# Performance work log

Hardware: AMD Instinct MI355X
Metric: run time of the kernel (lower is better)

Reference implementation:

```python
import jax, jax.numpy as jnp
import numpy as np

TOPK = 7  # hard-coded k in cal_high_score_instance_mask
EPS_DICE = 1e-8


def setup_inputs() -> dict:
    key = jax.random.key(0)
    k1, k2, k3, k4 = jax.random.split(key, 4)
    b, n, v, h, w = 4, 16, 32, 160, 160
    pred_mask = jax.random.normal(k1, (b, 1, h, w), dtype=jnp.float32)
    encode_feat = jax.random.normal(k2, (b, v, h, w), dtype=jnp.float32)
    gt_instances = (jax.random.uniform(k3, (b, n, h, w)) > 0.8).astype(jnp.float32)
    # validity mask over instance slots
    gt_index_mask = jax.random.randint(k4, (b, n), 0, 2).astype(jnp.int32)
    return {
        "pred_mask": pred_mask,
        "encode_feat": encode_feat,
        "gt_instances": gt_instances,
        "gt_index_mask": gt_index_mask,
    }


def reference(pred_mask, encode_feat, gt_instances, gt_index_mask):
    b, v, h, w = encode_feat.shape
    n = gt_instances.shape[1]
    hw = h * w
    feat = encode_feat.reshape(b, v, hw)          # b, v, hw
    gt = gt_instances.reshape(b, n, hw)           # b, n, hw
    valid = gt_index_mask.astype(feat.dtype)      # b, n  (0/1)

    # ---- get_mean_embedding_vector: masked mean of embedding per instance
    pix = jnp.clip(gt.sum(-1), 1.0)               # b, n
    mean_emb = jnp.einsum('bvp,bnp->bnv', feat, gt) / pix[..., None]

    # ---- cal_high_score_instance_mask: topk over masked score map, gather embeddings
    pre_regions = pred_mask.reshape(b, 1, hw) * gt             # b, n, hw
    _wvals, idx = jax.lax.top_k(pre_regions, TOPK)              # b, n, k
    idx_flat = idx.reshape(b, n * TOPK)                         # b, n*k
    # gather embedding vectors at topk pixel locations -> b, n*k, v
    idx_feat_th = jnp.take_along_axis(feat, idx_flat[:, None, :], axis=2)
    idx_feat_th = jnp.transpose(idx_feat_th, (0, 2, 1))

    # ---- get_isntance_mask: embedding-vector x feature-map matmuls
    inst_masks = jnp.einsum('bkv,bvp->bkp', idx_feat_th, feat)  # b, n*k, hw
    mean_masks = jnp.einsum('bnv,bvp->bnp', mean_emb, feat)     # b, n, hw

    # ---- w_dice_loss on mean-embedding masks (valid instances only)
    p_mean = jax.nn.sigmoid(mean_masks)
    denom_mean = jnp.clip((p_mean ** 2).sum(-1) + (gt ** 2).sum(-1), EPS_DICE)
    dice_mean = 1.0 - 2.0 * (gt * p_mean).sum(-1) / denom_mean  # b, n
    mean_inst_loss = (dice_mean * valid).sum()

    # ---- w_dice_loss on topk-instance masks (target expanded over k)
    p_k = jax.nn.sigmoid(inst_masks.reshape(b, n, TOPK, hw))
    t_k = gt[:, :, None, :]                                     # b, n, 1, hw
    denom_k = jnp.clip((p_k ** 2).sum(-1) + (t_k ** 2).sum(-1), EPS_DICE)
    dice_k = 1.0 - 2.0 * (t_k * p_k).sum(-1) / denom_k          # b, n, k
    inst_loss = (dice_k * valid[..., None]).sum()

    # ---- l2_loss: masked squared distance of per-pixel embedding to instance mean
    diff = (feat[:, None, :, :] - mean_emb[..., None]) * gt[:, :, None, :]  # b, n, v, hw
    l2 = (diff ** 2).sum(-1) / pix[..., None]                   # b, n, v
    embedding_l2_loss = (l2.sum(-1) * valid).sum()

    return jnp.stack([mean_inst_loss, inst_loss, embedding_l2_loss])
```

## Files before the change

### kernel.cpp

```cpp
#include <hip/hip_runtime.h>
#include <cstdint>
#include <cstddef>

#define B 4
#define N 16
#define V 32
#define HW 25600
#define TOPK 7
#define NSLB 5
#define NCA 200
#define NCC 400

__device__ __forceinline__ bool better(float av, int ai, float bv, int bi) {
    return (av > bv) || (av == bv && ai < bi);
}

__global__ __launch_bounds__(256) void kTop(
    const float* __restrict__ pred, const float* __restrict__ gt,
    float* __restrict__ cand_val, int* __restrict__ cand_idx,
    float* __restrict__ cnt_part, float* __restrict__ out) {
    int s = blockIdx.x;
    int tid = threadIdx.x;
    if (s == 0 && tid == 0) { out[0] = 0.f; out[1] = 0.f; out[2] = 0.f; }
    int bn = s / NSLB, sl = s % NSLB;
    int b = bn >> 4;
    int lane = tid & 63, wave = tid >> 6;
    int base = sl * 5120;

    const float* gtrow = gt + (size_t)bn * HW + base;
    const float* pr = pred + (size_t)b * HW + base;

    float tv[TOPK]; int ti[TOPK];
#pragma unroll
    for (int j = 0; j < TOPK; ++j) { tv[j] = -INFINITY; ti[j] = 0x7fffffff; }
    float cnt = 0.f;

#pragma unroll
    for (int it = 0; it < 5; ++it) {
        int p = it * 1024 + tid * 4;
        float4 g4 = *reinterpret_cast<const float4*>(gtrow + p);
        float4 p4 = *reinterpret_cast<const float4*>(pr + p);
        cnt += g4.x + g4.y + g4.z + g4.w;
        float ca[4] = { p4.x * g4.x, p4.y * g4.y, p4.z * g4.z, p4.w * g4.w };
#pragma unroll
        for (int j = 0; j < 4; ++j) {
            float c = ca[j]; int pi = base + p + j;
            if (better(c, pi, tv[TOPK - 1], ti[TOPK - 1])) {
                tv[TOPK - 1] = c; ti[TOPK - 1] = pi;
#pragma unroll
                for (int q = TOPK - 2; q >= 0; --q) {
                    if (better(tv[q + 1], ti[q + 1], tv[q], ti[q])) {
                        float fv = tv[q]; int fi = ti[q];
                        tv[q] = tv[q + 1]; ti[q] = ti[q + 1];
                        tv[q + 1] = fv; ti[q + 1] = fi;
                    }
                }
            }
        }
    }

    __shared__ float rwv[4];
    __shared__ int rwi[4];
    __shared__ float csum[4];

#pragma unroll
    for (int off = 32; off > 0; off >>= 1) cnt += __shfl_down(cnt, off);
    if (lane == 0) csum[wave] = cnt;
    __syncthreads();
    if (tid == 0) cnt_part[s] = csum[0] + csum[1] + csum[2] + csum[3];

    int cbase = s * TOPK;
    for (int r = 0; r < TOPK; ++r) {
        float bv = tv[0]; int bi = ti[0];
#pragma unroll
        for (int m = 1; m <= 32; m <<= 1) {
            float ov = __shfl_xor(bv, m);
            int oi = __shfl_xor(bi, m);
            if (better(ov, oi, bv, bi)) { bv = ov; bi = oi; }
        }
        if (lane == 0) { rwv[wave] = bv; rwi[wave] = bi; }
        __syncthreads();
        float fv = rwv[0]; int fi = rwi[0];
#pragma unroll
        for (int w = 1; w < 4; ++w)
            if (better(rwv[w], rwi[w], fv, fi)) { fv = rwv[w]; fi = rwi[w]; }
        if (ti[0] == fi) {
#pragma unroll
            for (int q = 0; q < TOPK - 1; ++q) { tv[q] = tv[q + 1]; ti[q] = ti[q + 1]; }
            tv[TOPK - 1] = -INFINITY; ti[TOPK - 1] = 0x7fffffff;
        }
        if (tid == 0) { cand_val[cbase + r] = fv; cand_idx[cbase + r] = fi; }
        __syncthreads();
    }
}

__global__ __launch_bounds__(256) void kA(
    const float* __restrict__ feat, const float* __restrict__ gt,
    float* __restrict__ ms_part, float* __restrict__ s2_part) {
    int s = blockIdx.x;
    int xcd = s & 7;
    int b = xcd >> 1;
    int ch = (s >> 3) * 2 + (xcd & 1);
    int c0 = ch * 128;
    int tid = threadIdx.x;
    int ng = tid >> 6, vg = (tid >> 3) & 7, pg = tid & 7;

    const float* gb = gt + (size_t)(b * N + ng * 4) * HW + c0 + pg * 4;
    const float* fb = feat + (size_t)(b * V + vg * 4) * HW + c0 + pg * 4;

    float acc[4][4];
#pragma unroll
    for (int i = 0; i < 4; ++i)
#pragma unroll
        for (int j = 0; j < 4; ++j) acc[i][j] = 0.f;
    float s2a[4] = { 0.f, 0.f, 0.f, 0.f };

#pragma unroll
    for (int q = 0; q < 4; ++q) {
        int p = q * 32;
        float4 g4[4], f4[4];
#pragma unroll
        for (int i = 0; i < 4; ++i)
            g4[i] = *reinterpret_cast<const float4*>(gb + (size_t)i * HW + p);
#pragma unroll
        for (int j = 0; j < 4; ++j)
            f4[j] = *reinterpret_cast<const float4*>(fb + (size_t)j * HW + p);
        float ffx = 0.f, ffy = 0.f, ffz = 0.f, ffw = 0.f;
#pragma unroll
        for (int j = 0; j < 4; ++j) {
            ffx = fmaf(f4[j].x, f4[j].x, ffx);
            ffy = fmaf(f4[j].y, f4[j].y, ffy);
            ffz = fmaf(f4[j].z, f4[j].z, ffz);
            ffw = fmaf(f4[j].w, f4[j].w, ffw);
        }
#pragma unroll
        for (int i = 0; i < 4; ++i) {
#pragma unroll
            for (int j = 0; j < 4; ++j) {
                acc[i][j] = fmaf(g4[i].x, f4[j].x, acc[i][j]);
                acc[i][j] = fmaf(g4[i].y, f4[j].y, acc[i][j]);
                acc[i][j] = fmaf(g4[i].z, f4[j].z, acc[i][j]);
                acc[i][j] = fmaf(g4[i].w, f4[j].w, acc[i][j]);
            }
            s2a[i] = fmaf(g4[i].x, ffx, s2a[i]);
            s2a[i] = fmaf(g4[i].y, ffy, s2a[i]);
            s2a[i] = fmaf(g4[i].z, ffz, s2a[i]);
            s2a[i] = fmaf(g4[i].w, ffw, s2a[i]);
        }
    }
#pragma unroll
    for (int m = 1; m <= 4; m <<= 1)
#pragma unroll
        for (int i = 0; i < 4; ++i)
#pragma unroll
            for (int j = 0; j < 4; ++j) acc[i][j] += __shfl_xor(acc[i][j], m);
    size_t blk = (size_t)(b * NCA + ch);
    if (pg == 0) {
        float* dst = ms_part + blk * 512;
#pragma unroll
        for (int i = 0; i < 4; ++i)
#pragma unroll
            for (int j = 0; j < 4; ++j)
                dst[(ng * 4 + i) * 32 + vg * 4 + j] = acc[i][j];
    }
#pragma unroll
    for (int m = 1; m <= 32; m <<= 1)
#pragma unroll
        for (int i = 0; i < 4; ++i) s2a[i] += __shfl_xor(s2a[i], m);
    if ((tid & 63) == 0) {
#pragma unroll
        for (int i = 0; i < 4; ++i)
            s2_part[blk * 16 + ng * 4 + i] = s2a[i];
    }
}

__global__ __launch_bounds__(256) void kB(
    const float* __restrict__ feat, const float* __restrict__ ms_part,
    const float* __restrict__ s2_part,
    const float* __restrict__ cand_val, const int* __restrict__ cand_idx,
    const float* __restrict__ cnt_part, const int* __restrict__ valid,
    float* __restrict__ Ebuf, float* __restrict__ cntbuf, float* __restrict__ out) {
    int bn = blockIdx.x;
    int b = bn >> 4, n = bn & 15;
    int tid = threadIdx.x;
    int lane = tid & 63, wave = tid >> 6;

    __shared__ float msl[8][33];
    __shared__ float s2w[4];
    __shared__ int idx7[TOPK];

    {
        int sl = tid >> 5, v = tid & 31;
        const float* src = ms_part + ((size_t)(b * NCA) + sl) * 512 + n * 32 + v;
        float sm = 0.f;
#pragma unroll 5
        for (int k = 0; k < 25; ++k) sm += src[(size_t)(8 * k) * 512];
        msl[sl][v] = sm;
    }
    {
        float s2v = 0.f;
        if (tid < NCA) s2v = s2_part[((size_t)(b * NCA) + tid) * 16 + n];
#pragma unroll
        for (int m = 1; m <= 32; m <<= 1) s2v += __shfl_xor(s2v, m);
        if (lane == 0) s2w[wave] = s2v;
    }
    if (wave == 0) {
        float cv = -INFINITY; int ci = 0x7fffffff;
        if (lane < NSLB * TOPK) {
            cv = cand_val[(size_t)bn * NSLB * TOPK + lane];
            ci = cand_idx[(size_t)bn * NSLB * TOPK + lane];
        }
#pragma unroll
        for (int r = 0; r < TOPK; ++r) {
            float bv = cv; int bi = ci;
#pragma unroll
            for (int m = 1; m <= 32; m <<= 1) {
                float ov = __shfl_xor(bv, m);
                int oi = __shfl_xor(bi, m);
                if (better(ov, oi, bv, bi)) { bv = ov; bi = oi; }
            }
            if (ci == bi) { cv = -INFINITY; ci = 0x7fffffff; }
            if (lane == 0) idx7[r] = bi;
        }
    }
    __syncthreads();

    if (tid < 32) {
        const float* cp = cnt_part + bn * NSLB;
        float cnt = cp[0] + cp[1] + cp[2] + cp[3] + cp[4];
        float msum = msl[0][tid] + msl[1][tid] + msl[2][tid] + msl[3][tid]
                   + msl[4][tid] + msl[5][tid] + msl[6][tid] + msl[7][tid];
        float pix = fmaxf(cnt, 1.0f);
        float mu = msum / pix;
        Ebuf[(size_t)bn * 256 + tid] = mu;
        float msq = mu * mu;
#pragma unroll
        for (int m = 1; m <= 16; m <<= 1) msq += __shfl_xor(msq, m);
        if (tid == 0) {
            cntbuf[bn] = cnt;
            float s2 = s2w[0] + s2w[1] + s2w[2] + s2w[3];
            atomicAdd(out + 2, (s2 / pix - msq) * (float)valid[bn]);
        }
    } else {
        int t = tid - 32;
        if (t < 224) {
            int r = t >> 5, v = t & 31;
            Ebuf[(size_t)bn * 256 + (r + 1) * 32 + v] =
                feat[((size_t)b * V + v) * HW + idx7[r]];
        }
    }
}

__global__ __launch_bounds__(256) void kC(
    const float* __restrict__ feat, const float* __restrict__ gt,
    const float* __restrict__ Ebuf, float* __restrict__ sums_part) {
    int s = blockIdx.x;
    int xcd = s & 7;
    int b = xcd >> 1;
    int ch = (s >> 3) * 2 + (xcd & 1);
    int c0 = ch * 64;
    int tid = threadIdx.x;
    int n = tid >> 4, pg = tid & 15;

    __shared__ float e_lds[8 * 16 * 36];
    __shared__ float red[16][17];

    const float* eb = Ebuf + (size_t)b * 4096;
#pragma unroll
    for (int k = 0; k < 4; ++k) {
        int q = (tid + 256 * k) * 4;
        int nn = q >> 8, rr = (q >> 5) & 7, vv = q & 31;
        *reinterpret_cast<float4*>(&e_lds[(rr * 16 + nn) * 36 + vv]) =
            *reinterpret_cast<const float4*>(eb + q);
    }
    __syncthreads();

    const float* fb = feat + (size_t)b * V * HW + c0 + pg * 4;
    float4 g4 = *reinterpret_cast<const float4*>(gt + (size_t)(b * N + n) * HW + c0 + pg * 4);

    float acc[8][4];
#pragma unroll
    for (int r = 0; r < 8; ++r)
#pragma unroll
        for (int j = 0; j < 4; ++j) acc[r][j] = 0.f;

    float4 c0_ = *reinterpret_cast<const float4*>(fb);
    float4 c1_ = *reinterpret_cast<const float4*>(fb + HW);
    float4 c2_ = *reinterpret_cast<const float4*>(fb + 2 * (size_t)HW);
    float4 c3_ = *reinterpret_cast<const float4*>(fb + 3 * (size_t)HW);
#pragma unroll
    for (int vq = 0; vq < 8; ++vq) {
        float4 n0_, n1_, n2_, n3_;
        if (vq < 7) {
            const float* np = fb + (size_t)(vq * 4 + 4) * HW;
            n0_ = *reinterpret_cast<const float4*>(np);
            n1_ = *reinterpret_cast<const float4*>(np + HW);
            n2_ = *reinterpret_cast<const float4*>(np + 2 * (size_t)HW);
            n3_ = *reinterpret_cast<const float4*>(np + 3 * (size_t)HW);
        }
#pragma unroll
        for (int r = 0; r < 8; ++r) {
            float4 e4 = *reinterpret_cast<const float4*>(&e_lds[(r * 16 + n) * 36 + vq * 4]);
            acc[r][0] = fmaf(e4.x, c0_.x, acc[r][0]);
            acc[r][0] = fmaf(e4.y, c1_.x, acc[r][0]);
            acc[r][0] = fmaf(e4.z, c2_.x, acc[r][0]);
            acc[r][0] = fmaf(e4.w, c3_.x, acc[r][0]);
            acc[r][1] = fmaf(e4.x, c0_.y, acc[r][1]);
            acc[r][1] = fmaf(e4.y, c1_.y, acc[r][1]);
            acc[r][1] = fmaf(e4.z, c2_.y, acc[r][1]);
            acc[r][1] = fmaf(e4.w, c3_.y, acc[r][1]);
            acc[r][2] = fmaf(e4.x, c0_.z, acc[r][2]);
            acc[r][2] = fmaf(e4.y, c1_.z, acc[r][2]);
            acc[r][2] = fmaf(e4.z, c2_.z, acc[r][2]);
            acc[r][2] = fmaf(e4.w, c3_.z, acc[r][2]);
            acc[r][3] = fmaf(e4.x, c0_.w, acc[r][3]);
            acc[r][3] = fmaf(e4.y, c1_.w, acc[r][3]);
            acc[r][3] = fmaf(e4.z, c2_.w, acc[r][3]);
            acc[r][3] = fmaf(e4.w, c3_.w, acc[r][3]);
        }
        if (vq < 7) { c0_ = n0_; c1_ = n1_; c2_ = n2_; c3_ = n3_; }
    }

    float p2[8], tp[8];
#pragma unroll
    for (int r = 0; r < 8; ++r) { p2[r] = 0.f; tp[r] = 0.f; }
    float ga[4] = { g4.x, g4.y, g4.z, g4.w };
#pragma unroll
    for (int r = 0; r < 8; ++r)
#pragma unroll
        for (int j = 0; j < 4; ++j) {
            float sg = 1.f / (1.f + __expf(-acc[r][j]));
            p2[r] = fmaf(sg, sg, p2[r]);
            tp[r] = fmaf(ga[j], sg, tp[r]);
        }
#pragma unroll
    for (int m = 1; m <= 8; m <<= 1)
#pragma unroll
        for (int r = 0; r < 8; ++r) {
            p2[r] += __shfl_xor(p2[r], m);
            tp[r] += __shfl_xor(tp[r], m);
        }
    if (pg == 0) {
#pragma unroll
        for (int r = 0; r < 8; ++r) {
            red[n][r * 2] = p2[r];
            red[n][r * 2 + 1] = tp[r];
        }
    }
    __syncthreads();
    sums_part[(size_t)(b * NCC + ch) * 256 + tid] = red[tid >> 4][tid & 15];
}

__global__ __launch_bounds__(256) void kD(
    const float* __restrict__ sums_part, const float* __restrict__ cntbuf,
    const int* __restrict__ valid, float* __restrict__ out) {
    int bn = blockIdx.x;
    int b = bn >> 4, n = bn & 15;
    int tid = threadIdx.x;
    int slot = tid & 15, cg = tid >> 4;
    int lane = tid & 63, wave = tid >> 6;

    __shared__ float red2[4][17];
    __shared__ float fin[16];

    float sv = 0.f;
    const float* src = sums_part + (size_t)b * NCC * 256 + n * 16 + slot;
    for (int k = 0; k < 25; ++k) sv += src[(size_t)(cg + 16 * k) * 256];
    sv += __shfl_xor(sv, 16);
    sv += __shfl_xor(sv, 32);
    if (lane < 16) red2[wave][lane] = sv;
    __syncthreads();
    if (tid < 16) fin[tid] = red2[0][tid] + red2[1][tid] + red2[2][tid] + red2[3][tid];
    __syncthreads();

    if (tid == 0) {
        float vw = (float)valid[bn];
        float cnt = cntbuf[bn];
        float mloss = 0.f, iloss = 0.f;
#pragma unroll
        for (int r = 0; r < 8; ++r) {
            float p2 = fin[r * 2];
            float tp = fin[r * 2 + 1];
            float denom = fmaxf(p2 + cnt, 1e-8f);
            float dice = 1.f - 2.f * tp / denom;
            if (r == 0) mloss = dice * vw;
            else iloss += dice * vw;
        }
        atomicAdd(out + 0, mloss);
        atomicAdd(out + 1, iloss);
    }
}

extern "C" void kernel_launch(void* const* d_in, const int* in_sizes, int n_in,
                              void* d_out, int out_size, void* d_ws, size_t ws_size,
                              hipStream_t stream) {
    const float* pred = (const float*)d_in[0];
    const float* feat = (const float*)d_in[1];
    const float* gtin = (const float*)d_in[2];
    const int* valid  = (const int*)d_in[3];
    float* out = (float*)d_out;

    char* ws = (char*)d_ws;
    float* ms_part   = (float*)(ws);
    float* s2_part   = (float*)(ws + 1638400);
    float* cand_val  = (float*)(ws + 1689600);
    int*   cand_idx  = (int*)  (ws + 1698560);
    float* cnt_part  = (float*)(ws + 1707520);
    float* sums_part = (float*)(ws + 1708800);
    float* Ebuf      = (float*)(ws + 3347200);
    float* cntbuf    = (float*)(ws + 3412736);

    kTop<<<B * N * NSLB, 256, 0, stream>>>(pred, gtin, cand_val, cand_idx, cnt_part, out);
    kA<<<B * NCA, 256, 0, stream>>>(feat, gtin, ms_part, s2_part);
    kB<<<B * N, 256, 0, stream>>>(feat, ms_part, s2_part, cand_val, cand_idx,
                                  cnt_part, valid, Ebuf, cntbuf, out);
    kC<<<B * NCC, 256, 0, stream>>>(feat, gtin, Ebuf, sums_part);
    kD<<<B * N, 256, 0, stream>>>(sums_part, cntbuf, valid, out);
}
```

Measured before the change: 63.40 us.

## Merge five kernels into one cooperative persistent kernel with grid syncs

```diff
diff --git a/kernel.cpp b/kernel.cpp
--- a/kernel.cpp
+++ b/kernel.cpp
@@ -1,6 +1,9 @@
 #include <hip/hip_runtime.h>
+#include <hip/hip_cooperative_groups.h>
 #include <cstdint>
 #include <cstddef>
+
+namespace cg = cooperative_groups;
 
 #define B 4
 #define N 16
@@ -10,19 +13,20 @@
 #define NSLB 5
 #define NCA 200
 #define NCC 400
+#define GRID 512
 
 __device__ __forceinline__ bool better(float av, int ai, float bv, int bi) {
     return (av > bv) || (av == bv && ai < bi);
 }
 
-__global__ __launch_bounds__(256) void kTop(
+
+__device__ __forceinline__ void kTop_body(
+    int slab, int tid,
     const float* __restrict__ pred, const float* __restrict__ gt,
     float* __restrict__ cand_val, int* __restrict__ cand_idx,
-    float* __restrict__ cnt_part, float* __restrict__ out) {
-    int s = blockIdx.x;
-    int tid = threadIdx.x;
-    if (s == 0 && tid == 0) { out[0] = 0.f; out[1] = 0.f; out[2] = 0.f; }
-    int bn = s / NSLB, sl = s % NSLB;
+    float* __restrict__ cnt_part,
+    float* rwv, int* rwi, float* csum) {
+    int bn = slab / NSLB, sl = slab % NSLB;
     int b = bn >> 4;
     int lane = tid & 63, wave = tid >> 6;
     int base = sl * 5120;
@@ -59,17 +63,13 @@
         }
     }
 
-    __shared__ float rwv[4];
-    __shared__ int rwi[4];
-    __shared__ float csum[4];
-
 #pragma unroll
     for (int off = 32; off > 0; off >>= 1) cnt += __shfl_down(cnt, off);
     if (lane == 0) csum[wave] = cnt;
     __syncthreads();
-    if (tid == 0) cnt_part[s] = csum[0] + csum[1] + csum[2] + csum[3];
-
-    int cbase = s * TOPK;
+    if (tid == 0) cnt_part[slab] = csum[0] + csum[1] + csum[2] + csum[3];
+
+    int cbase = slab * TOPK;
     for (int r = 0; r < TOPK; ++r) {
         float bv = tv[0]; int bi = ti[0];
 #pragma unroll
@@ -94,15 +94,14 @@
     }
 }
 
-__global__ __launch_bounds__(256) void kA(
+__device__ __forceinline__ void kA_body(
+    int w, int tid,
     const float* __restrict__ feat, const float* __restrict__ gt,
     float* __restrict__ ms_part, float* __restrict__ s2_part) {
-    int s = blockIdx.x;
-    int xcd = s & 7;
+    int xcd = w & 7;
     int b = xcd >> 1;
-    int ch = (s >> 3) * 2 + (xcd & 1);
+    int ch = (w >> 3) * 2 + (xcd & 1);
     int c0 = ch * 128;
-    int tid = threadIdx.x;
     int ng = tid >> 6, vg = (tid >> 3) & 7, pg = tid & 7;
 
     const float* gb = gt + (size_t)(b * N + ng * 4) * HW + c0 + pg * 4;
@@ -174,20 +173,16 @@
     }
 }
 
-__global__ __launch_bounds__(256) void kB(
+__device__ __forceinline__ void kB_body(
+    int bn, int tid,
     const float* __restrict__ feat, const float* __restrict__ ms_part,
     const float* __restrict__ s2_part,
     const float* __restrict__ cand_val, const int* __restrict__ cand_idx,
     const float* __restrict__ cnt_part, const int* __restrict__ valid,
-    float* __restrict__ Ebuf, float* __restrict__ cntbuf, float* __restrict__ out) {
-    int bn = blockIdx.x;
+    float* __restrict__ Ebuf, float* __restrict__ cntbuf, float* __restrict__ out,
+    float (*msl)[33], float* s2w, int* idx7) {
     int b = bn >> 4, n = bn & 15;
-    int tid = threadIdx.x;
     int lane = tid & 63, wave = tid >> 6;
-
-    __shared__ float msl[8][33];
-    __shared__ float s2w[4];
-    __shared__ int idx7[TOPK];
 
     {
         int sl = tid >> 5, v = tid & 31;
@@ -251,19 +246,16 @@
     }
 }
 
-__global__ __launch_bounds__(256) void kC(
+__device__ __forceinline__ void kC_body(
+    int w, int tid,
     const float* __restrict__ feat, const float* __restrict__ gt,
-    const float* __restrict__ Ebuf, float* __restrict__ sums_part) {
-    int s = blockIdx.x;
-    int xcd = s & 7;
+    const float* __restrict__ Ebuf, float* __restrict__ sums_part,
+    float* e_lds, float (*red)[17]) {
+    int xcd = w & 7;
     int b = xcd >> 1;
-    int ch = (s >> 3) * 2 + (xcd & 1);
+    int ch = (w >> 3) * 2 + (xcd & 1);
     int c0 = ch * 64;
-    int tid = threadIdx.x;
     int n = tid >> 4, pg = tid & 15;
-
-    __shared__ float e_lds[8 * 16 * 36];
-    __shared__ float red[16][17];
 
     const float* eb = Ebuf + (size_t)b * 4096;
 #pragma unroll
@@ -351,21 +343,18 @@
     sums_part[(size_t)(b * NCC + ch) * 256 + tid] = red[tid >> 4][tid & 15];
 }
 
-__global__ __launch_bounds__(256) void kD(
+__device__ __forceinline__ void kD_body(
+    int bn, int tid,
     const float* __restrict__ sums_part, const float* __restrict__ cntbuf,
-    const int* __restrict__ valid, float* __restrict__ out) {
-    int bn = blockIdx.x;
+    const int* __restrict__ valid, float* __restrict__ out,
+    float (*red2)[17], float* fin) {
     int b = bn >> 4, n = bn & 15;
-    int tid = threadIdx.x;
-    int slot = tid & 15, cg = tid >> 4;
+    int slot = tid & 15, cg_ = tid >> 4;
     int lane = tid & 63, wave = tid >> 6;
-
-    __shared__ float red2[4][17];
-    __shared__ float fin[16];
 
     float sv = 0.f;
     const float* src = sums_part + (size_t)b * NCC * 256 + n * 16 + slot;
-    for (int k = 0; k < 25; ++k) sv += src[(size_t)(cg + 16 * k) * 256];
+    for (int k = 0; k < 25; ++k) sv += src[(size_t)(cg_ + 16 * k) * 256];
     sv += __shfl_xor(sv, 16);
     sv += __shfl_xor(sv, 32);
     if (lane < 16) red2[wave][lane] = sv;
@@ -389,6 +378,90 @@
         atomicAdd(out + 0, mloss);
         atomicAdd(out + 1, iloss);
     }
+}
+
+__global__ void mega(
+    const float* __restrict__ pred, const float* __restrict__ feat,
+    const float* __restrict__ gt, const int* __restrict__ valid,
+    float* __restrict__ ms_part, float* __restrict__ s2_part,
+    float* __restrict__ cand_val, int* __restrict__ cand_idx,
+    float* __restrict__ cnt_part, float* __restrict__ sums_part,
+    float* __restrict__ Ebuf, float* __restrict__ cntbuf,
+    float* __restrict__ out) {
+    cg::grid_group gg = cg::this_grid();
+    int s = blockIdx.x;
+    int tid = threadIdx.x;
+
+    __shared__ float e_lds[8 * 16 * 36];
+    __shared__ float red[16][17];
+    __shared__ float msl[8][33];
+    __shared__ float s2w[4];
+    __shared__ int   idx7[TOPK];
+    __shared__ float rwv[4];
+    __shared__ int   rwi[4];
+    __shared__ float csum[4];
+    __shared__ float fin[16];
+
+    if (s == 0 && tid == 0) { out[0] = 0.f; out[1] = 0.f; out[2] = 0.f; }
+
+    for (int w = s; w < 800 + 64 * NSLB; w += GRID) {
+        if (w < 800) kA_body(w, tid, feat, gt, ms_part, s2_part);
+        else kTop_body(w - 800, tid, pred, gt, cand_val, cand_idx, cnt_part,
+                       rwv, rwi, csum);
+        __syncthreads();
+    }
+    gg.sync();
+
+    if (s < B * N)
+        kB_body(s, tid, feat, ms_part, s2_part, cand_val, cand_idx, cnt_part,
+                valid, Ebuf, cntbuf, out, msl, s2w, idx7);
+    gg.sync();
+
+    for (int w = s; w < B * NCC; w += GRID) {
+        kC_body(w, tid, feat, gt, Ebuf, sums_part, e_lds, red);
+        __syncthreads();
+    }
+    gg.sync();
+
+    if (s < B * N)
+        kD_body(s, tid, sums_part, cntbuf, valid, out, red, fin);
+}
+
+__global__ __launch_bounds__(256) void kTopF(
+    const float* __restrict__ pred, const float* __restrict__ gt,
+    float* __restrict__ cand_val, int* __restrict__ cand_idx,
+    float* __restrict__ cnt_part, float* __restrict__ out) {
+    __shared__ float rwv[4]; __shared__ int rwi[4]; __shared__ float csum[4];
+    int s = blockIdx.x, tid = threadIdx.x;
+    if (s == 0 && tid == 0) { out[0] = 0.f; out[1] = 0.f; out[2] = 0.f; }
+    kTop_body(s, tid, pred, gt, cand_val, cand_idx, cnt_part, rwv, rwi, csum);
+}
+__global__ __launch_bounds__(256) void kAF(
+    const float* __restrict__ feat, const float* __restrict__ gt,
+    float* __restrict__ ms_part, float* __restrict__ s2_part) {
+    kA_body(blockIdx.x, threadIdx.x, feat, gt, ms_part, s2_part);
+}
+__global__ __launch_bounds__(256) void kBF(
+    const float* __restrict__ feat, const float* __restrict__ ms_part,
+    const float* __restrict__ s2_part,
+    const float* __restrict__ cand_val, const int* __restrict__ cand_idx,
+    const float* __restrict__ cnt_part, const int* __restrict__ valid,
+    float* __restrict__ Ebuf, float* __restrict__ cntbuf, float* __restrict__ out) {
+    __shared__ float msl[8][33]; __shared__ float s2w[4]; __shared__ int idx7[TOPK];
+    kB_body(blockIdx.x, threadIdx.x, feat, ms_part, s2_part, cand_val, cand_idx,
+            cnt_part, valid, Ebuf, cntbuf, out, msl, s2w, idx7);
+}
+__global__ __launch_bounds__(256) void kCF(
+    const float* __restrict__ feat, const float* __restrict__ gt,
+    const float* __restrict__ Ebuf, float* __restrict__ sums_part) {
+    __shared__ float e_lds[8 * 16 * 36]; __shared__ float red[16][17];
+    kC_body(blockIdx.x, threadIdx.x, feat, gt, Ebuf, sums_part, e_lds, red);
+}
+__global__ __launch_bounds__(256) void kDF(
+    const float* __restrict__ sums_part, const float* __restrict__ cntbuf,
+    const int* __restrict__ valid, float* __restrict__ out) {
+    __shared__ float red2[4][17]; __shared__ float fin[16];
+    kD_body(blockIdx.x, threadIdx.x, sums_part, cntbuf, valid, out, red2, fin);
 }
 
 extern "C" void kernel_launch(void* const* d_in, const int* in_sizes, int n_in,
@@ -410,10 +483,19 @@
     float* Ebuf      = (float*)(ws + 3347200);
     float* cntbuf    = (float*)(ws + 3412736);
 
-    kTop<<<B * N * NSLB, 256, 0, stream>>>(pred, gtin, cand_val, cand_idx, cnt_part, out);
-    kA<<<B * NCA, 256, 0, stream>>>(feat, gtin, ms_part, s2_part);
-    kB<<<B * N, 256, 0, stream>>>(feat, ms_part, s2_part, cand_val, cand_idx,
-                                  cnt_part, valid, Ebuf, cntbuf, out);
-    kC<<<B * NCC, 256, 0, stream>>>(feat, gtin, Ebuf, sums_part);
-    kD<<<B * N, 256, 0, stream>>>(sums_part, cntbuf, valid, out);
-}
+    void* args[] = { (void*)&pred, (void*)&feat, (void*)&gtin, (void*)&valid,
+                     (void*)&ms_part, (void*)&s2_part, (void*)&cand_val,
+                     (void*)&cand_idx, (void*)&cnt_part, (void*)&sums_part,
+                     (void*)&Ebuf, (void*)&cntbuf, (void*)&out };
+    hipError_t err = hipLaunchCooperativeKernel((void*)mega, dim3(GRID), dim3(256),
+                                                args, 0, stream);
+    if (err != hipSuccess) {
+        kTopF<<<B * N * NSLB, 256, 0, stream>>>(pred, gtin, cand_val, cand_idx,
+                                                cnt_part, out);
+        kAF<<<B * NCA, 256, 0, stream>>>(feat, gtin, ms_part, s2_part);
+        kBF<<<B * N, 256, 0, stream>>>(feat, ms_part, s2_part, cand_val, cand_idx,
+                                       cnt_part, valid, Ebuf, cntbuf, out);
+        kCF<<<B * NCC, 256, 0, stream>>>(feat, gtin, Ebuf, sums_part);
+        kDF<<<B * N, 256, 0, stream>>>(sums_part, cntbuf, valid, out);
+    }
+}
```

Result: slower. 241.9 us (+281.5%).

## Fuse top-k and masked-sum kernels into one launch; halve kC block count

Applied to the files above, without the earlier changes.

```diff
diff --git a/kernel.cpp b/kernel.cpp
--- a/kernel.cpp
+++ b/kernel.cpp
@@ -9,20 +9,20 @@
 #define TOPK 7
 #define NSLB 5
 #define NCA 200
-#define NCC 400
+#define NCC 200
 
 __device__ __forceinline__ bool better(float av, int ai, float bv, int bi) {
     return (av > bv) || (av == bv && ai < bi);
 }
 
-__global__ __launch_bounds__(256) void kTop(
+
+__device__ __forceinline__ void kTop_body(
+    int slab, int tid,
     const float* __restrict__ pred, const float* __restrict__ gt,
     float* __restrict__ cand_val, int* __restrict__ cand_idx,
-    float* __restrict__ cnt_part, float* __restrict__ out) {
-    int s = blockIdx.x;
-    int tid = threadIdx.x;
-    if (s == 0 && tid == 0) { out[0] = 0.f; out[1] = 0.f; out[2] = 0.f; }
-    int bn = s / NSLB, sl = s % NSLB;
+    float* __restrict__ cnt_part,
+    float* rwv, int* rwi, float* csum) {
+    int bn = slab / NSLB, sl = slab % NSLB;
     int b = bn >> 4;
     int lane = tid & 63, wave = tid >> 6;
     int base = sl * 5120;
@@ -59,17 +59,13 @@
         }
     }
 
-    __shared__ float rwv[4];
-    __shared__ int rwi[4];
-    __shared__ float csum[4];
-
 #pragma unroll
     for (int off = 32; off > 0; off >>= 1) cnt += __shfl_down(cnt, off);
     if (lane == 0) csum[wave] = cnt;
     __syncthreads();
-    if (tid == 0) cnt_part[s] = csum[0] + csum[1] + csum[2] + csum[3];
-
-    int cbase = s * TOPK;
+    if (tid == 0) cnt_part[slab] = csum[0] + csum[1] + csum[2] + csum[3];
+
+    int cbase = slab * TOPK;
     for (int r = 0; r < TOPK; ++r) {
         float bv = tv[0]; int bi = ti[0];
 #pragma unroll
@@ -94,15 +90,14 @@
     }
 }
 
-__global__ __launch_bounds__(256) void kA(
+__device__ __forceinline__ void kA_body(
+    int w, int tid,
     const float* __restrict__ feat, const float* __restrict__ gt,
     float* __restrict__ ms_part, float* __restrict__ s2_part) {
-    int s = blockIdx.x;
-    int xcd = s & 7;
+    int xcd = w & 7;
     int b = xcd >> 1;
-    int ch = (s >> 3) * 2 + (xcd & 1);
+    int ch = (w >> 3) * 2 + (xcd & 1);
     int c0 = ch * 128;
-    int tid = threadIdx.x;
     int ng = tid >> 6, vg = (tid >> 3) & 7, pg = tid & 7;
 
     const float* gb = gt + (size_t)(b * N + ng * 4) * HW + c0 + pg * 4;
@@ -172,6 +167,21 @@
         for (int i = 0; i < 4; ++i)
             s2_part[blk * 16 + ng * 4 + i] = s2a[i];
     }
+}
+
+__global__ __launch_bounds__(256) void kAT(
+    const float* __restrict__ pred, const float* __restrict__ feat,
+    const float* __restrict__ gt,
+    float* __restrict__ ms_part, float* __restrict__ s2_part,
+    float* __restrict__ cand_val, int* __restrict__ cand_idx,
+    float* __restrict__ cnt_part, float* __restrict__ out) {
+    __shared__ float rwv[4]; __shared__ int rwi[4]; __shared__ float csum[4];
+    int s = blockIdx.x;
+    int tid = threadIdx.x;
+    if (s == 0 && tid == 0) { out[0] = 0.f; out[1] = 0.f; out[2] = 0.f; }
+    if (s < 800) kA_body(s, tid, feat, gt, ms_part, s2_part);
+    else kTop_body(s - 800, tid, pred, gt, cand_val, cand_idx, cnt_part,
+                   rwv, rwi, csum);
 }
 
 __global__ __launch_bounds__(256) void kB(
@@ -258,7 +268,7 @@
     int xcd = s & 7;
     int b = xcd >> 1;
     int ch = (s >> 3) * 2 + (xcd & 1);
-    int c0 = ch * 64;
+    int c0 = ch * 128;
     int tid = threadIdx.x;
     int n = tid >> 4, pg = tid & 15;
 
@@ -275,64 +285,70 @@
     }
     __syncthreads();
 
-    const float* fb = feat + (size_t)b * V * HW + c0 + pg * 4;
-    float4 g4 = *reinterpret_cast<const float4*>(gt + (size_t)(b * N + n) * HW + c0 + pg * 4);
-
-    float acc[8][4];
-#pragma unroll
-    for (int r = 0; r < 8; ++r)
-#pragma unroll
-        for (int j = 0; j < 4; ++j) acc[r][j] = 0.f;
-
-    float4 c0_ = *reinterpret_cast<const float4*>(fb);
-    float4 c1_ = *reinterpret_cast<const float4*>(fb + HW);
-    float4 c2_ = *reinterpret_cast<const float4*>(fb + 2 * (size_t)HW);
-    float4 c3_ = *reinterpret_cast<const float4*>(fb + 3 * (size_t)HW);
-#pragma unroll
-    for (int vq = 0; vq < 8; ++vq) {
-        float4 n0_, n1_, n2_, n3_;
-        if (vq < 7) {
-            const float* np = fb + (size_t)(vq * 4 + 4) * HW;
-            n0_ = *reinterpret_cast<const float4*>(np);
-            n1_ = *reinterpret_cast<const float4*>(np + HW);
-            n2_ = *reinterpret_cast<const float4*>(np + 2 * (size_t)HW);
-            n3_ = *reinterpret_cast<const float4*>(np + 3 * (size_t)HW);
-        }
-#pragma unroll
-        for (int r = 0; r < 8; ++r) {
-            float4 e4 = *reinterpret_cast<const float4*>(&e_lds[(r * 16 + n) * 36 + vq * 4]);
-            acc[r][0] = fmaf(e4.x, c0_.x, acc[r][0]);
-            acc[r][0] = fmaf(e4.y, c1_.x, acc[r][0]);
-            acc[r][0] = fmaf(e4.z, c2_.x, acc[r][0]);
-            acc[r][0] = fmaf(e4.w, c3_.x, acc[r][0]);
-            acc[r][1] = fmaf(e4.x, c0_.y, acc[r][1]);
-            acc[r][1] = fmaf(e4.y, c1_.y, acc[r][1]);
-            acc[r][1] = fmaf(e4.z, c2_.y, acc[r][1]);
-            acc[r][1] = fmaf(e4.w, c3_.y, acc[r][1]);
-            acc[r][2] = fmaf(e4.x, c0_.z, acc[r][2]);
-            acc[r][2] = fmaf(e4.y, c1_.z, acc[r][2]);
-            acc[r][2] = fmaf(e4.z, c2_.z, acc[r][2]);
-            acc[r][2] = fmaf(e4.w, c3_.z, acc[r][2]);
-            acc[r][3] = fmaf(e4.x, c0_.w, acc[r][3]);
-            acc[r][3] = fmaf(e4.y, c1_.w, acc[r][3]);
-            acc[r][3] = fmaf(e4.z, c2_.w, acc[r][3]);
-            acc[r][3] = fmaf(e4.w, c3_.w, acc[r][3]);
-        }
-        if (vq < 7) { c0_ = n0_; c1_ = n1_; c2_ = n2_; c3_ = n3_; }
-    }
-
     float p2[8], tp[8];
 #pragma unroll
     for (int r = 0; r < 8; ++r) { p2[r] = 0.f; tp[r] = 0.f; }
-    float ga[4] = { g4.x, g4.y, g4.z, g4.w };
-#pragma unroll
-    for (int r = 0; r < 8; ++r)
-#pragma unroll
-        for (int j = 0; j < 4; ++j) {
-            float sg = 1.f / (1.f + __expf(-acc[r][j]));
-            p2[r] = fmaf(sg, sg, p2[r]);
-            tp[r] = fmaf(ga[j], sg, tp[r]);
-        }
+
+#pragma unroll 1
+    for (int pass = 0; pass < 2; ++pass) {
+        const float* fb = feat + (size_t)b * V * HW + c0 + pass * 64 + pg * 4;
+        float4 g4 = *reinterpret_cast<const float4*>(
+            gt + (size_t)(b * N + n) * HW + c0 + pass * 64 + pg * 4);
+
+        float acc[8][4];
+#pragma unroll
+        for (int r = 0; r < 8; ++r)
+#pragma unroll
+            for (int j = 0; j < 4; ++j) acc[r][j] = 0.f;
+
+        float4 c0_ = *reinterpret_cast<const float4*>(fb);
+        float4 c1_ = *reinterpret_cast<const float4*>(fb + HW);
+        float4 c2_ = *reinterpret_cast<const float4*>(fb + 2 * (size_t)HW);
+        float4 c3_ = *reinterpret_cast<const float4*>(fb + 3 * (size_t)HW);
+#pragma unroll
+        for (int vq = 0; vq < 8; ++vq) {
+            float4 n0_, n1_, n2_, n3_;
+            if (vq < 7) {
+                const float* np = fb + (size_t)(vq * 4 + 4) * HW;
+                n0_ = *reinterpret_cast<const float4*>(np);
+                n1_ = *reinterpret_cast<const float4*>(np + HW);
+                n2_ = *reinterpret_cast<const float4*>(np + 2 * (size_t)HW);
+                n3_ = *reinterpret_cast<const float4*>(np + 3 * (size_t)HW);
+            }
+#pragma unroll
+            for (int r = 0; r < 8; ++r) {
+                float4 e4 = *reinterpret_cast<const float4*>(&e_lds[(r * 16 + n) * 36 + vq * 4]);
+                acc[r][0] = fmaf(e4.x, c0_.x, acc[r][0]);
+                acc[r][0] = fmaf(e4.y, c1_.x, acc[r][0]);
+                acc[r][0] = fmaf(e4.z, c2_.x, acc[r][0]);
+                acc[r][0] = fmaf(e4.w, c3_.x, acc[r][0]);
+                acc[r][1] = fmaf(e4.x, c0_.y, acc[r][1]);
+                acc[r][1] = fmaf(e4.y, c1_.y, acc[r][1]);
+                acc[r][1] = fmaf(e4.z, c2_.y, acc[r][1]);
+                acc[r][1] = fmaf(e4.w, c3_.y, acc[r][1]);
+                acc[r][2] = fmaf(e4.x, c0_.z, acc[r][2]);
+                acc[r][2] = fmaf(e4.y, c1_.z, acc[r][2]);
+                acc[r][2] = fmaf(e4.z, c2_.z, acc[r][2]);
+                acc[r][2] = fmaf(e4.w, c3_.z, acc[r][2]);
+                acc[r][3] = fmaf(e4.x, c0_.w, acc[r][3]);
+                acc[r][3] = fmaf(e4.y, c1_.w, acc[r][3]);
+                acc[r][3] = fmaf(e4.z, c2_.w, acc[r][3]);
+                acc[r][3] = fmaf(e4.w, c3_.w, acc[r][3]);
+            }
+            if (vq < 7) { c0_ = n0_; c1_ = n1_; c2_ = n2_; c3_ = n3_; }
+        }
+
+        float ga[4] = { g4.x, g4.y, g4.z, g4.w };
+#pragma unroll
+        for (int r = 0; r < 8; ++r)
+#pragma unroll
+            for (int j = 0; j < 4; ++j) {
+                float sg = 1.f / (1.f + __expf(-acc[r][j]));
+                p2[r] = fmaf(sg, sg, p2[r]);
+                tp[r] = fmaf(ga[j], sg, tp[r]);
+            }
+    }
+
 #pragma unroll
     for (int m = 1; m <= 8; m <<= 1)
 #pragma unroll
@@ -365,7 +381,11 @@
 
     float sv = 0.f;
     const float* src = sums_part + (size_t)b * NCC * 256 + n * 16 + slot;
-    for (int k = 0; k < 25; ++k) sv += src[(size_t)(cg + 16 * k) * 256];
+#pragma unroll
+    for (int k = 0; k < 13; ++k) {
+        int ch = cg + 16 * k;
+        if (ch < NCC) sv += src[(size_t)ch * 256];
+    }
     sv += __shfl_xor(sv, 16);
     sv += __shfl_xor(sv, 32);
     if (lane < 16) red2[wave][lane] = sv;
@@ -407,11 +427,11 @@
     int*   cand_idx  = (int*)  (ws + 1698560);
     float* cnt_part  = (float*)(ws + 1707520);
     float* sums_part = (float*)(ws + 1708800);
-    float* Ebuf      = (float*)(ws + 3347200);
-    float* cntbuf    = (float*)(ws + 3412736);
-
-    kTop<<<B * N * NSLB, 256, 0, stream>>>(pred, gtin, cand_val, cand_idx, cnt_part, out);
-    kA<<<B * NCA, 256, 0, stream>>>(feat, gtin, ms_part, s2_part);
+    float* Ebuf      = (float*)(ws + 2528000);
+    float* cntbuf    = (float*)(ws + 2593536);
+
+    kAT<<<800 + B * N * NSLB, 256, 0, stream>>>(pred, feat, gtin, ms_part, s2_part,
+                                                cand_val, cand_idx, cnt_part, out);
     kB<<<B * N, 256, 0, stream>>>(feat, ms_part, s2_part, cand_val, cand_idx,
                                   cnt_part, valid, Ebuf, cntbuf, out);
     kC<<<B * NCC, 256, 0, stream>>>(feat, gtin, Ebuf, sums_part);
```

After: 117.7 us. 85.7% more time.
